# Performance work log

Measured on AMD Instinct MI355X. Metric: run time of the kernel, lower is better.

## Reference

```python
import jax, jax.numpy as jnp
import numpy as np

S, D_IN, N_RULES, N_OUT = 8192, 1024, 16, 512  # batch, in_features, num_rules, out_features


def setup_inputs() -> dict:
    key = jax.random.key(0)
    k1, k2, k3, k4 = jax.random.split(key, 4)
    X = jax.random.normal(k1, (S, D_IN), dtype=jnp.float32)
    # fc layer weight/bias after add_neurons: out_features = N_RULES * N_OUT
    W = jax.random.normal(k2, (N_RULES * N_OUT, D_IN), dtype=jnp.float32) / np.sqrt(D_IN).astype(np.float32)
    b = jax.random.normal(k3, (N_RULES * N_OUT,), dtype=jnp.float32) * 0.01
    # rule firing strengths from Layer (computed under no_grad in the original)
    lambdas = jax.random.uniform(k4, (S, N_RULES), dtype=jnp.float32)
    return {"X": X, "W": W, "b": b, "lambdas": lambdas}


def reference(X, W, b, lambdas):
    # X: [S, D_IN]; W: [R*O, D_IN]; b: [R*O]; lambdas: [S, R]
    H = jax.nn.sigmoid(X @ W.T + b)                       # [S, R*O]
    Hr = H.reshape(H.shape[0], lambdas.shape[1], N_OUT)   # [S, R, O] (block n = cols n*O:(n+1)*O)
    # apply_rule_strength: out[s,o] = sum_r lambdas[s,r] * H[s, r*O + o]
    return jnp.einsum('sr,sro->so', lambdas, Hr)          # [S, O]
```

## Files before the change

### kernel.cpp

```cpp
#include <hip/hip_runtime.h>
#include <hip/hip_bf16.h>
#include <stdint.h>

#define SS 8192
#define DD 1024
#define RR 16
#define OO 512

typedef __bf16 bf16_8 __attribute__((ext_vector_type(8)));
typedef float f32_4 __attribute__((ext_vector_type(4)));
typedef int i32_4 __attribute__((ext_vector_type(4)));

typedef __attribute__((address_space(1))) void g1_void;
typedef __attribute__((address_space(3))) void lds_void;

#define L2E 1.44269504f

__device__ __forceinline__ void gload_lds16(const void* g, void* l) {
  __builtin_amdgcn_global_load_lds((g1_void*)(uintptr_t)g,
                                   (lds_void*)(uint32_t)(uintptr_t)l, 16, 0, 0);
}

__global__ __launch_bounds__(256) void somfnn_quant(
    const float* __restrict__ X, const float* __restrict__ W,
    char* __restrict__ Xq, char* __restrict__ Wq,
    float* __restrict__ sX, float* __restrict__ sW, float4* __restrict__ out) {
  const int tid = threadIdx.x;
  const int wv = tid >> 6;
  const int l = tid & 63;
  const int r = blockIdx.x * 4 + wv;
  const bool isX = r < SS;
  const float* src = isX ? (X + (size_t)r * DD) : (W + (size_t)(r - SS) * DD);
  char* dst = isX ? (Xq + (size_t)r * DD) : (Wq + (size_t)(r - SS) * DD);

  const float4* s4 = (const float4*)src;
  float4 v[4];
#pragma unroll
  for (int c = 0; c < 4; ++c) v[c] = s4[c * 64 + l];

  out[(size_t)blockIdx.x * 256 + tid] = float4{0.f, 0.f, 0.f, 0.f};

  float m = 0.f;
#pragma unroll
  for (int c = 0; c < 4; ++c)
    m = fmaxf(m, fmaxf(fmaxf(fabsf(v[c].x), fabsf(v[c].y)),
                       fmaxf(fabsf(v[c].z), fabsf(v[c].w))));
#pragma unroll
  for (int off = 32; off > 0; off >>= 1) m = fmaxf(m, __shfl_xor(m, off, 64));
  m = fmaxf(m, 1e-20f);

  const float inv = 127.0f / m;
  int* di = (int*)dst;
#pragma unroll
  for (int c = 0; c < 4; ++c) {
    int q0 = __float2int_rn(v[c].x * inv);
    int q1 = __float2int_rn(v[c].y * inv);
    int q2 = __float2int_rn(v[c].z * inv);
    int q3 = __float2int_rn(v[c].w * inv);
    di[c * 64 + l] = (q0 & 0xff) | ((q1 & 0xff) << 8) | ((q2 & 0xff) << 16) |
                     ((q3 & 0xff) << 24);
  }
  if (l == 0) {
    if (isX) sX[r] = m / 127.0f;
    else sW[r - SS] = m / 127.0f;
  }
}

__global__ __launch_bounds__(256, 2) void somfnn_gemm_i8(
    const char* __restrict__ Xq, const char* __restrict__ Wq,
    const float* __restrict__ sX, const float* __restrict__ sW,
    const float* __restrict__ bias_g, const float* __restrict__ lam_g,
    float* __restrict__ out) {
  constexpr int BM = 128, BN = 128, BK = 128;
  constexpr int TILEB = BM * BK;
  constexpr int NSTEP = 8 * (DD / BK);

  __shared__ __align__(16) char lds_a[2][TILEB];
  __shared__ __align__(16) char lds_b[2][TILEB];
  __shared__ float lds_bias[8 * BN];
  __shared__ float lds_lam[8 * BM];
  __shared__ float lds_sB[8 * BN];
  __shared__ float lds_sA[BM];

  const int tid = threadIdx.x;
  const int bid = blockIdx.x;

  const int l = tid & 63;
  const int w = tid >> 6;
  const int lane15 = l & 15;
  const int q = l >> 4;
  const int wm = w >> 1;
  const int wn = w & 1;

  const int xcd = bid & 7;
  const int chunk = bid >> 3;
  const int sb = xcd * 8 + (chunk & 7);
  const int ob = (chunk >> 3) & 3;
  const int rhalf = chunk >> 5;
  const int s0 = sb * BM;
  const int o0 = ob * BN;
  const int r0 = rhalf * 8;

  for (int idx = tid; idx < 8 * BN; idx += 256) {
    int rr = idx >> 7, j = idx & 127;
    lds_bias[idx] = -L2E * bias_g[(r0 + rr) * OO + o0 + j];
    lds_sB[idx] = sW[(r0 + rr) * OO + o0 + j];
  }
  for (int idx = tid; idx < 8 * BM; idx += 256) {
    int rr = idx >> 7, i = idx & 127;
    lds_lam[idx] = lam_g[(s0 + i) * RR + (r0 + rr)];
  }
  if (tid < BM) lds_sA[tid] = sX[s0 + tid];

  int goffs[4];
#pragma unroll
  for (int i = 0; i < 4; ++i) {
    int c = (w * 4 + i) * 64 + l;
    int row = c >> 3;
    int k16 = (c & 7) ^ (row & 7);
    goffs[i] = row * DD + k16 * 16;
  }

  int afo[4], bfo[4];
#pragma unroll
  for (int t = 0; t < 4; ++t) {
    int ra = wm * 64 + t * 16 + lane15;
    afo[t] = ra * BK + ((q ^ (ra & 7)) * 16);
    int rb = wn * 64 + t * 16 + lane15;
    bfo[t] = rb * BK + ((q ^ (rb & 7)) * 16);
  }

  auto issue_pre = [&](int step, int buf) {
    int rl = step >> 3, kt = step & 7;
    const char* ga = Xq + (size_t)s0 * DD + kt * BK;
    const char* gb = Wq + ((size_t)(r0 + rl) * OO + o0) * DD + kt * BK;
#pragma unroll
    for (int i = 0; i < 4; ++i)
      gload_lds16(ga + goffs[i], &lds_a[buf][(w * 4 + i) * 1024]);
#pragma unroll
    for (int i = 0; i < 4; ++i)
      gload_lds16(gb + goffs[i], &lds_b[buf][(w * 4 + i) * 1024]);
  };

  i32_4 acc[4][4];
  f32_4 oacc[4][4];
#pragma unroll
  for (int mi = 0; mi < 4; ++mi)
#pragma unroll
    for (int ni = 0; ni < 4; ++ni) {
      acc[mi][ni] = i32_4{0, 0, 0, 0};
      oacc[mi][ni] = f32_4{0.f, 0.f, 0.f, 0.f};
    }

  issue_pre(0, 0);
  __syncthreads();

  for (int step = 0; step < NSTEP; ++step) {
    const int cur = step & 1;
    const bool more = (step + 1) < NSTEP;
    if (more) issue_pre(step + 1, cur ^ 1);

    const char* A = lds_a[cur];
    const char* B = lds_b[cur];
#pragma unroll
    for (int ks = 0; ks < 2; ++ks) {
      const int xr = ks ? 64 : 0;
      i32_4 av[4], bv[4];
#pragma unroll
      for (int mi = 0; mi < 4; ++mi) av[mi] = *(const i32_4*)(A + (afo[mi] ^ xr));
#pragma unroll
      for (int ni = 0; ni < 4; ++ni) bv[ni] = *(const i32_4*)(B + (bfo[ni] ^ xr));
#pragma unroll
      for (int mi = 0; mi < 4; ++mi)
#pragma unroll
        for (int ni = 0; ni < 4; ++ni)
          acc[mi][ni] =
              __builtin_amdgcn_mfma_i32_16x16x64_i8(av[mi], bv[ni], acc[mi][ni], 0, 0, 0);
    }

    if ((step & 7) == 7) {
      const int rl = step >> 3;
      float lsa[4][4], lamv[4][4];
#pragma unroll
      for (int mi = 0; mi < 4; ++mi)
#pragma unroll
        for (int v = 0; v < 4; ++v) {
          int ridx = wm * 64 + mi * 16 + q * 4 + v;
          lsa[mi][v] = -L2E * lds_sA[ridx];
          lamv[mi][v] = lds_lam[rl * BM + ridx];
        }
#pragma unroll
      for (int ni = 0; ni < 4; ++ni) {
        const int cidx = wn * 64 + ni * 16 + lane15;
        const float nb = lds_bias[rl * BN + cidx];
        const float sbv = lds_sB[rl * BN + cidx];
#pragma unroll
        for (int mi = 0; mi < 4; ++mi)
#pragma unroll
          for (int v = 0; v < 4; ++v) {
            float t = __builtin_fmaf((float)acc[mi][ni][v], lsa[mi][v] * sbv, nb);
            float e = __builtin_amdgcn_exp2f(t);
            float h = __builtin_amdgcn_rcpf(1.0f + e);
            oacc[mi][ni][v] = __builtin_fmaf(lamv[mi][v], h, oacc[mi][ni][v]);
            acc[mi][ni][v] = 0;
          }
      }
    }
    __syncthreads();
  }

#pragma unroll
  for (int mi = 0; mi < 4; ++mi)
#pragma unroll
    for (int ni = 0; ni < 4; ++ni)
#pragma unroll
      for (int v = 0; v < 4; ++v) {
        int row = s0 + wm * 64 + mi * 16 + q * 4 + v;
        int col = o0 + wn * 64 + ni * 16 + lane15;
        atomicAdd(&out[row * OO + col], oacc[mi][ni][v]);
      }
}

__global__ __launch_bounds__(256, 2) void somfnn_gemm_fb(
    const float* __restrict__ Xf32, const float* __restrict__ Wf32,
    const float* __restrict__ bias_g, const float* __restrict__ lam_g,
    float* __restrict__ out) {
  constexpr int BM = 128, BN = 128, BK = 64;
  constexpr int TILE = BM * BK;
  constexpr int NSTEP = 8 * (DD / BK);

  __shared__ __align__(16) __bf16 lds_a[2][TILE];
  __shared__ __align__(16) __bf16 lds_b[2][TILE];
  __shared__ float lds_bias[8 * BN];
  __shared__ float lds_lam[8 * BM];

  const int tid = threadIdx.x;
  const int bid = blockIdx.x;
  const int l = tid & 63;
  const int w = tid >> 6;
  const int lane15 = l & 15;
  const int q = l >> 4;
  const int wm = w >> 1;
  const int wn = w & 1;

  const int xcd = bid & 7;
  const int chunk = bid >> 3;
  const int sb = xcd * 8 + (chunk & 7);
  const int ob = (chunk >> 3) & 3;
  const int rhalf = chunk >> 5;
  const int s0 = sb * BM;
  const int o0 = ob * BN;
  const int r0 = rhalf * 8;

  for (int idx = tid; idx < 8 * BN; idx += 256) {
    int rr = idx >> 7, j = idx & 127;
    lds_bias[idx] = -L2E * bias_g[(r0 + rr) * OO + o0 + j];
  }
  for (int idx = tid; idx < 8 * BM; idx += 256) {
    int rr = idx >> 7, i = idx & 127;
    lds_lam[idx] = lam_g[(s0 + i) * RR + (r0 + rr)];
  }

  int goffs[4], coffs[4];
#pragma unroll
  for (int i = 0; i < 4; ++i) {
    int c = (w * 4 + i) * 64 + l;
    int row = c >> 3;
    int k8 = (c & 7) ^ (row & 7);
    goffs[i] = row * DD + k8 * 8;
    coffs[i] = c * 8;
  }
  int afo[4], bfo[4];
#pragma unroll
  for (int t = 0; t < 4; ++t) {
    int ra = wm * 64 + t * 16 + lane15;
    afo[t] = (ra * 8 + (q ^ (ra & 7))) * 8;
    int rb = wn * 64 + t * 16 + lane15;
    bfo[t] = (rb * 8 + (q ^ (rb & 7))) * 8;
  }

  float4 ra_[4][2], rb_[4][2];
  auto issue_fb = [&](int step) {
    int rl = step >> 4, kt = step & 15;
    const float* ga = Xf32 + s0 * DD + kt * BK;
    const float* gb = Wf32 + ((r0 + rl) * OO + o0) * DD + kt * BK;
#pragma unroll
    for (int i = 0; i < 4; ++i) {
      const float4* p = (const float4*)(ga + goffs[i]);
      ra_[i][0] = p[0]; ra_[i][1] = p[1];
      const float4* pb = (const float4*)(gb + goffs[i]);
      rb_[i][0] = pb[0]; rb_[i][1] = pb[1];
    }
  };
  auto commit_fb = [&](int buf) {
#pragma unroll
    for (int i = 0; i < 4; ++i) {
      bf16_8 t;
      t[0] = (__bf16)ra_[i][0].x; t[1] = (__bf16)ra_[i][0].y;
      t[2] = (__bf16)ra_[i][0].z; t[3] = (__bf16)ra_[i][0].w;
      t[4] = (__bf16)ra_[i][1].x; t[5] = (__bf16)ra_[i][1].y;
      t[6] = (__bf16)ra_[i][1].z; t[7] = (__bf16)ra_[i][1].w;
      *(bf16_8*)&lds_a[buf][coffs[i]] = t;
      bf16_8 u;
      u[0] = (__bf16)rb_[i][0].x; u[1] = (__bf16)rb_[i][0].y;
      u[2] = (__bf16)rb_[i][0].z; u[3] = (__bf16)rb_[i][0].w;
      u[4] = (__bf16)rb_[i][1].x; u[5] = (__bf16)rb_[i][1].y;
      u[6] = (__bf16)rb_[i][1].z; u[7] = (__bf16)rb_[i][1].w;
      *(bf16_8*)&lds_b[buf][coffs[i]] = u;
    }
  };

  f32_4 acc[4][4], oacc[4][4];
#pragma unroll
  for (int mi = 0; mi < 4; ++mi)
#pragma unroll
    for (int ni = 0; ni < 4; ++ni) {
      acc[mi][ni] = f32_4{0.f, 0.f, 0.f, 0.f};
      oacc[mi][ni] = f32_4{0.f, 0.f, 0.f, 0.f};
    }

  issue_fb(0);
  commit_fb(0);
  __syncthreads();

  for (int step = 0; step < NSTEP; ++step) {
    const int cur = step & 1;
    const bool more = (step + 1) < NSTEP;
    if (more) issue_fb(step + 1);

    const __bf16* A = lds_a[cur];
    const __bf16* B = lds_b[cur];
#pragma unroll
    for (int ks = 0; ks < 2; ++ks) {
      const int xr = ks ? 32 : 0;
      bf16_8 av[4], bv[4];
#pragma unroll
      for (int mi = 0; mi < 4; ++mi) av[mi] = *(const bf16_8*)(A + (afo[mi] ^ xr));
#pragma unroll
      for (int ni = 0; ni < 4; ++ni) bv[ni] = *(const bf16_8*)(B + (bfo[ni] ^ xr));
#pragma unroll
      for (int mi = 0; mi < 4; ++mi)
#pragma unroll
        for (int ni = 0; ni < 4; ++ni)
          acc[mi][ni] =
              __builtin_amdgcn_mfma_f32_16x16x32_bf16(av[mi], bv[ni], acc[mi][ni], 0, 0, 0);
    }
    if (more) commit_fb(cur ^ 1);

    if ((step & 15) == 15) {
      const int rl = step >> 4;
      float lamv[4][4];
#pragma unroll
      for (int mi = 0; mi < 4; ++mi)
#pragma unroll
        for (int v = 0; v < 4; ++v)
          lamv[mi][v] = lds_lam[rl * BM + wm * 64 + mi * 16 + q * 4 + v];
#pragma unroll
      for (int ni = 0; ni < 4; ++ni) {
        const float nb = lds_bias[rl * BN + wn * 64 + ni * 16 + lane15];
#pragma unroll
        for (int mi = 0; mi < 4; ++mi)
#pragma unroll
          for (int v = 0; v < 4; ++v) {
            float t = __builtin_fmaf(acc[mi][ni][v], -L2E, nb);
            float e = __builtin_amdgcn_exp2f(t);
            float h = __builtin_amdgcn_rcpf(1.0f + e);
            oacc[mi][ni][v] = __builtin_fmaf(lamv[mi][v], h, oacc[mi][ni][v]);
            acc[mi][ni][v] = 0.f;
          }
      }
    }
    __syncthreads();
  }

#pragma unroll
  for (int mi = 0; mi < 4; ++mi)
#pragma unroll
    for (int ni = 0; ni < 4; ++ni)
#pragma unroll
      for (int v = 0; v < 4; ++v) {
        int row = s0 + wm * 64 + mi * 16 + q * 4 + v;
        int col = o0 + wn * 64 + ni * 16 + lane15;
        atomicAdd(&out[row * OO + col], oacc[mi][ni][v]);
      }
}

extern "C" void kernel_launch(void* const* d_in, const int* in_sizes, int n_in,
                              void* d_out, int out_size, void* d_ws, size_t ws_size,
                              hipStream_t stream) {
  const float* X = (const float*)d_in[0];
  const float* W = (const float*)d_in[1];
  const float* b = (const float*)d_in[2];
  const float* lam = (const float*)d_in[3];
  float* out = (float*)d_out;

  const size_t qbytes = (size_t)SS * DD;
  const size_t need = 2 * qbytes + 2 * (size_t)SS * sizeof(float);
  if (ws_size >= need) {
    char* Xq = (char*)d_ws;
    char* Wq = Xq + qbytes;
    float* sX = (float*)(Wq + qbytes);
    float* sW = sX + SS;
    somfnn_quant<<<dim3(4096), dim3(256), 0, stream>>>(X, W, Xq, Wq, sX, sW, (float4*)out);
    somfnn_gemm_i8<<<dim3(512), dim3(256), 0, stream>>>(Xq, Wq, sX, sW, b, lam, out);
  } else {
    hipMemsetAsync(out, 0, (size_t)SS * OO * sizeof(float), stream);
    somfnn_gemm_fb<<<dim3(512), dim3(256), 0, stream>>>(X, W, b, lam, out);
  }
}
```

Baseline: 199.4 us.

## Reuse each X tile across two rules per K step with dual accumulators

The int8 GEMM now processes two rules at once. It loads one 64-wide K slice of the X tile and W tiles for two rules, then runs MFMAs into two separate accumulator sets. This halves how often the X tile is reloaded into LDS and held in registers across the 8 rules, at the cost of twice the accumulator registers and a new swizzle for the narrower BK. The added register pressure could spill or lower occupancy under launch_bounds(256,2).

```diff
diff --git a/kernel.cpp b/kernel.cpp
--- a/kernel.cpp
+++ b/kernel.cpp
@@ -71,12 +71,13 @@
     const float* __restrict__ sX, const float* __restrict__ sW,
     const float* __restrict__ bias_g, const float* __restrict__ lam_g,
     float* __restrict__ out) {
-  constexpr int BM = 128, BN = 128, BK = 128;
+  constexpr int BM = 128, BN = 128, BK = 64;
   constexpr int TILEB = BM * BK;
-  constexpr int NSTEP = 8 * (DD / BK);
+  constexpr int KT = DD / BK;
+  constexpr int NSTEP = 4 * KT;
 
   __shared__ __align__(16) char lds_a[2][TILEB];
-  __shared__ __align__(16) char lds_b[2][TILEB];
+  __shared__ __align__(16) char lds_b[2][2][TILEB];
   __shared__ float lds_bias[8 * BN];
   __shared__ float lds_lam[8 * BM];
   __shared__ float lds_sB[8 * BN];
@@ -112,48 +113,81 @@
   }
   if (tid < BM) lds_sA[tid] = sX[s0 + tid];
 
-  int goffs[4];
-#pragma unroll
-  for (int i = 0; i < 4; ++i) {
-    int c = (w * 4 + i) * 64 + l;
-    int row = c >> 3;
-    int k16 = (c & 7) ^ (row & 7);
-    goffs[i] = row * DD + k16 * 16;
+  int goffs[2];
+#pragma unroll
+  for (int i = 0; i < 2; ++i) {
+    int cc = (w * 2 + i) * 64 + l;
+    int row = cc >> 2;
+    int lc = cc & 3;
+    goffs[i] = row * DD + ((lc ^ ((row >> 1) & 3)) * 16);
   }
 
   int afo[4], bfo[4];
 #pragma unroll
   for (int t = 0; t < 4; ++t) {
     int ra = wm * 64 + t * 16 + lane15;
-    afo[t] = ra * BK + ((q ^ (ra & 7)) * 16);
+    afo[t] = ra * BK + ((q ^ ((ra >> 1) & 3)) * 16);
     int rb = wn * 64 + t * 16 + lane15;
-    bfo[t] = rb * BK + ((q ^ (rb & 7)) * 16);
+    bfo[t] = rb * BK + ((q ^ ((rb >> 1) & 3)) * 16);
   }
 
   auto issue_pre = [&](int step, int buf) {
-    int rl = step >> 3, kt = step & 7;
+    int rp = step >> 4, kt = step & 15;
     const char* ga = Xq + (size_t)s0 * DD + kt * BK;
-    const char* gb = Wq + ((size_t)(r0 + rl) * OO + o0) * DD + kt * BK;
-#pragma unroll
-    for (int i = 0; i < 4; ++i)
-      gload_lds16(ga + goffs[i], &lds_a[buf][(w * 4 + i) * 1024]);
-#pragma unroll
-    for (int i = 0; i < 4; ++i)
-      gload_lds16(gb + goffs[i], &lds_b[buf][(w * 4 + i) * 1024]);
+    const char* gb0 = Wq + ((size_t)(r0 + 2 * rp) * OO + o0) * DD + kt * BK;
+    const char* gb1 = gb0 + (size_t)OO * DD;
+#pragma unroll
+    for (int i = 0; i < 2; ++i)
+      gload_lds16(ga + goffs[i], &lds_a[buf][(w * 2 + i) * 1024]);
+#pragma unroll
+    for (int i = 0; i < 2; ++i)
+      gload_lds16(gb0 + goffs[i], &lds_b[buf][0][(w * 2 + i) * 1024]);
+#pragma unroll
+    for (int i = 0; i < 2; ++i)
+      gload_lds16(gb1 + goffs[i], &lds_b[buf][1][(w * 2 + i) * 1024]);
   };
 
-  i32_4 acc[4][4];
+  i32_4 acc0[4][4], acc1[4][4];
   f32_4 oacc[4][4];
 #pragma unroll
   for (int mi = 0; mi < 4; ++mi)
 #pragma unroll
     for (int ni = 0; ni < 4; ++ni) {
-      acc[mi][ni] = i32_4{0, 0, 0, 0};
+      acc0[mi][ni] = i32_4{0, 0, 0, 0};
+      acc1[mi][ni] = i32_4{0, 0, 0, 0};
       oacc[mi][ni] = f32_4{0.f, 0.f, 0.f, 0.f};
     }
 
   issue_pre(0, 0);
   __syncthreads();
+
+  auto do_epi = [&](i32_4 (&ac)[4][4], int rr) {
+    float lsa[4][4], lamv[4][4];
+#pragma unroll
+    for (int mi = 0; mi < 4; ++mi)
+#pragma unroll
+      for (int v = 0; v < 4; ++v) {
+        int ridx = wm * 64 + mi * 16 + q * 4 + v;
+        lsa[mi][v] = -L2E * lds_sA[ridx];
+        lamv[mi][v] = lds_lam[rr * BM + ridx];
+      }
+#pragma unroll
+    for (int ni = 0; ni < 4; ++ni) {
+      const int cidx = wn * 64 + ni * 16 + lane15;
+      const float nb = lds_bias[rr * BN + cidx];
+      const float sbv = lds_sB[rr * BN + cidx];
+#pragma unroll
+      for (int mi = 0; mi < 4; ++mi)
+#pragma unroll
+        for (int v = 0; v < 4; ++v) {
+          float t = __builtin_fmaf((float)ac[mi][ni][v], lsa[mi][v] * sbv, nb);
+          float e = __builtin_amdgcn_exp2f(t);
+          float h = __builtin_amdgcn_rcpf(1.0f + e);
+          oacc[mi][ni][v] = __builtin_fmaf(lamv[mi][v], h, oacc[mi][ni][v]);
+          ac[mi][ni][v] = 0;
+        }
+    }
+  };
 
   for (int step = 0; step < NSTEP; ++step) {
     const int cur = step & 1;
@@ -161,50 +195,33 @@
     if (more) issue_pre(step + 1, cur ^ 1);
 
     const char* A = lds_a[cur];
-    const char* B = lds_b[cur];
-#pragma unroll
-    for (int ks = 0; ks < 2; ++ks) {
-      const int xr = ks ? 64 : 0;
-      i32_4 av[4], bv[4];
-#pragma unroll
-      for (int mi = 0; mi < 4; ++mi) av[mi] = *(const i32_4*)(A + (afo[mi] ^ xr));
-#pragma unroll
-      for (int ni = 0; ni < 4; ++ni) bv[ni] = *(const i32_4*)(B + (bfo[ni] ^ xr));
-#pragma unroll
-      for (int mi = 0; mi < 4; ++mi)
-#pragma unroll
-        for (int ni = 0; ni < 4; ++ni)
-          acc[mi][ni] =
-              __builtin_amdgcn_mfma_i32_16x16x64_i8(av[mi], bv[ni], acc[mi][ni], 0, 0, 0);
-    }
-
-    if ((step & 7) == 7) {
-      const int rl = step >> 3;
-      float lsa[4][4], lamv[4][4];
-#pragma unroll
-      for (int mi = 0; mi < 4; ++mi)
-#pragma unroll
-        for (int v = 0; v < 4; ++v) {
-          int ridx = wm * 64 + mi * 16 + q * 4 + v;
-          lsa[mi][v] = -L2E * lds_sA[ridx];
-          lamv[mi][v] = lds_lam[rl * BM + ridx];
-        }
-#pragma unroll
-      for (int ni = 0; ni < 4; ++ni) {
-        const int cidx = wn * 64 + ni * 16 + lane15;
-        const float nb = lds_bias[rl * BN + cidx];
-        const float sbv = lds_sB[rl * BN + cidx];
-#pragma unroll
-        for (int mi = 0; mi < 4; ++mi)
-#pragma unroll
-          for (int v = 0; v < 4; ++v) {
-            float t = __builtin_fmaf((float)acc[mi][ni][v], lsa[mi][v] * sbv, nb);
-            float e = __builtin_amdgcn_exp2f(t);
-            float h = __builtin_amdgcn_rcpf(1.0f + e);
-            oacc[mi][ni][v] = __builtin_fmaf(lamv[mi][v], h, oacc[mi][ni][v]);
-            acc[mi][ni][v] = 0;
-          }
-      }
+    const char* B0 = lds_b[cur][0];
+    const char* B1 = lds_b[cur][1];
+
+    i32_4 av[4], bv[4];
+#pragma unroll
+    for (int mi = 0; mi < 4; ++mi) av[mi] = *(const i32_4*)(A + afo[mi]);
+#pragma unroll
+    for (int ni = 0; ni < 4; ++ni) bv[ni] = *(const i32_4*)(B0 + bfo[ni]);
+#pragma unroll
+    for (int mi = 0; mi < 4; ++mi)
+#pragma unroll
+      for (int ni = 0; ni < 4; ++ni)
+        acc0[mi][ni] =
+            __builtin_amdgcn_mfma_i32_16x16x64_i8(av[mi], bv[ni], acc0[mi][ni], 0, 0, 0);
+#pragma unroll
+    for (int ni = 0; ni < 4; ++ni) bv[ni] = *(const i32_4*)(B1 + bfo[ni]);
+#pragma unroll
+    for (int mi = 0; mi < 4; ++mi)
+#pragma unroll
+      for (int ni = 0; ni < 4; ++ni)
+        acc1[mi][ni] =
+            __builtin_amdgcn_mfma_i32_16x16x64_i8(av[mi], bv[ni], acc1[mi][ni], 0, 0, 0);
+
+    if ((step & 15) == 15) {
+      const int rp = step >> 4;
+      do_epi(acc0, 2 * rp);
+      do_epi(acc1, 2 * rp + 1);
     }
     __syncthreads();
   }
```

After: 197.9 us. Within noise of the previous version (-0.8%).

## Use triple-buffered BK=64 pipeline with partial vmcnt waits in int8 GEMM

Applied to the files above, without the earlier changes.

Halves the K tile to 64 and moves from double to triple buffering of the LDS tiles, issuing loads two steps ahead. The full __syncthreads is replaced by s_waitcnt vmcnt(4) plus a raw s_barrier, so the next stage's loads stay in flight across the barrier. The LDS swizzle is adjusted for the narrower 64-byte rows. The intent is to hide global-to-LDS latency better, at the cost of twice as many barriers and a smaller MFMA batch per step.

```diff
diff --git a/kernel.cpp b/kernel.cpp
--- a/kernel.cpp
+++ b/kernel.cpp
@@ -71,12 +71,12 @@
     const float* __restrict__ sX, const float* __restrict__ sW,
     const float* __restrict__ bias_g, const float* __restrict__ lam_g,
     float* __restrict__ out) {
-  constexpr int BM = 128, BN = 128, BK = 128;
+  constexpr int BM = 128, BN = 128, BK = 64;
   constexpr int TILEB = BM * BK;
   constexpr int NSTEP = 8 * (DD / BK);
 
-  __shared__ __align__(16) char lds_a[2][TILEB];
-  __shared__ __align__(16) char lds_b[2][TILEB];
+  __shared__ __align__(16) char lds_a[3][TILEB];
+  __shared__ __align__(16) char lds_b[3][TILEB];
   __shared__ float lds_bias[8 * BN];
   __shared__ float lds_lam[8 * BM];
   __shared__ float lds_sB[8 * BN];
@@ -112,34 +112,34 @@
   }
   if (tid < BM) lds_sA[tid] = sX[s0 + tid];
 
-  int goffs[4];
-#pragma unroll
-  for (int i = 0; i < 4; ++i) {
-    int c = (w * 4 + i) * 64 + l;
-    int row = c >> 3;
-    int k16 = (c & 7) ^ (row & 7);
-    goffs[i] = row * DD + k16 * 16;
+  int goffs[2];
+#pragma unroll
+  for (int i = 0; i < 2; ++i) {
+    int cc = (w * 2 + i) * 64 + l;
+    int row = cc >> 2;
+    int lc = cc & 3;
+    goffs[i] = row * DD + ((lc ^ ((row >> 1) & 3)) * 16);
   }
 
   int afo[4], bfo[4];
 #pragma unroll
   for (int t = 0; t < 4; ++t) {
     int ra = wm * 64 + t * 16 + lane15;
-    afo[t] = ra * BK + ((q ^ (ra & 7)) * 16);
+    afo[t] = ra * BK + ((q ^ ((ra >> 1) & 3)) * 16);
     int rb = wn * 64 + t * 16 + lane15;
-    bfo[t] = rb * BK + ((q ^ (rb & 7)) * 16);
+    bfo[t] = rb * BK + ((q ^ ((rb >> 1) & 3)) * 16);
   }
 
   auto issue_pre = [&](int step, int buf) {
-    int rl = step >> 3, kt = step & 7;
+    int rl = step >> 4, kt = step & 15;
     const char* ga = Xq + (size_t)s0 * DD + kt * BK;
     const char* gb = Wq + ((size_t)(r0 + rl) * OO + o0) * DD + kt * BK;
 #pragma unroll
-    for (int i = 0; i < 4; ++i)
-      gload_lds16(ga + goffs[i], &lds_a[buf][(w * 4 + i) * 1024]);
-#pragma unroll
-    for (int i = 0; i < 4; ++i)
-      gload_lds16(gb + goffs[i], &lds_b[buf][(w * 4 + i) * 1024]);
+    for (int i = 0; i < 2; ++i)
+      gload_lds16(ga + goffs[i], &lds_a[buf][(w * 2 + i) * 1024]);
+#pragma unroll
+    for (int i = 0; i < 2; ++i)
+      gload_lds16(gb + goffs[i], &lds_b[buf][(w * 2 + i) * 1024]);
   };
 
   i32_4 acc[4][4];
@@ -152,34 +152,35 @@
       oacc[mi][ni] = f32_4{0.f, 0.f, 0.f, 0.f};
     }
 
+  asm volatile("s_waitcnt vmcnt(0)" ::: "memory");
   issue_pre(0, 0);
-  __syncthreads();
+  issue_pre(1, 1);
+  asm volatile("s_waitcnt vmcnt(4) lgkmcnt(0)" ::: "memory");
+  __builtin_amdgcn_sched_barrier(0);
+  __builtin_amdgcn_s_barrier();
+  __builtin_amdgcn_sched_barrier(0);
 
   for (int step = 0; step < NSTEP; ++step) {
-    const int cur = step & 1;
-    const bool more = (step + 1) < NSTEP;
-    if (more) issue_pre(step + 1, cur ^ 1);
+    const int cur = step % 3;
+    const bool more = (step + 2) < NSTEP;
+    if (more) issue_pre(step + 2, (step + 2) % 3);
 
     const char* A = lds_a[cur];
     const char* B = lds_b[cur];
-#pragma unroll
-    for (int ks = 0; ks < 2; ++ks) {
-      const int xr = ks ? 64 : 0;
-      i32_4 av[4], bv[4];
-#pragma unroll
-      for (int mi = 0; mi < 4; ++mi) av[mi] = *(const i32_4*)(A + (afo[mi] ^ xr));
-#pragma unroll
-      for (int ni = 0; ni < 4; ++ni) bv[ni] = *(const i32_4*)(B + (bfo[ni] ^ xr));
-#pragma unroll
-      for (int mi = 0; mi < 4; ++mi)
-#pragma unroll
-        for (int ni = 0; ni < 4; ++ni)
-          acc[mi][ni] =
-              __builtin_amdgcn_mfma_i32_16x16x64_i8(av[mi], bv[ni], acc[mi][ni], 0, 0, 0);
-    }
-
-    if ((step & 7) == 7) {
-      const int rl = step >> 3;
+    i32_4 av[4], bv[4];
+#pragma unroll
+    for (int mi = 0; mi < 4; ++mi) av[mi] = *(const i32_4*)(A + afo[mi]);
+#pragma unroll
+    for (int ni = 0; ni < 4; ++ni) bv[ni] = *(const i32_4*)(B + bfo[ni]);
+#pragma unroll
+    for (int mi = 0; mi < 4; ++mi)
+#pragma unroll
+      for (int ni = 0; ni < 4; ++ni)
+        acc[mi][ni] =
+            __builtin_amdgcn_mfma_i32_16x16x64_i8(av[mi], bv[ni], acc[mi][ni], 0, 0, 0);
+
+    if ((step & 15) == 15) {
+      const int rl = step >> 4;
       float lsa[4][4], lamv[4][4];
 #pragma unroll
       for (int mi = 0; mi < 4; ++mi)
@@ -206,7 +207,15 @@
           }
       }
     }
-    __syncthreads();
+
+    if (more) {
+      asm volatile("s_waitcnt vmcnt(4) lgkmcnt(0)" ::: "memory");
+    } else {
+      asm volatile("s_waitcnt vmcnt(0) lgkmcnt(0)" ::: "memory");
+    }
+    __builtin_amdgcn_sched_barrier(0);
+    __builtin_amdgcn_s_barrier();
+    __builtin_amdgcn_sched_barrier(0);
   }
 
 #pragma unroll
```

Result: slower. 204.4 us (+2.5%).

## Give each wave private LDS tiles and drop block-wide barriers in int8 GEMM loop

Applied to the files above, without the earlier changes.

The int8 GEMM now has each wave load its own 64-row A and B slices into a private double-buffered LDS region, with BK shrunk to 64. The per-step __syncthreads is replaced by explicit vmcnt/lgkmcnt waits, so waves run independently and keep two loads in flight. The aim is to remove block-wide barrier stalls and overlap loads with MFMA. In exchange, the four waves no longer share loads, so global/L2 traffic per block roughly doubles, and correctness depends on the hand-written waitcnt ordering.

```diff
diff --git a/kernel.cpp b/kernel.cpp
--- a/kernel.cpp
+++ b/kernel.cpp
@@ -71,12 +71,10 @@
     const float* __restrict__ sX, const float* __restrict__ sW,
     const float* __restrict__ bias_g, const float* __restrict__ lam_g,
     float* __restrict__ out) {
-  constexpr int BM = 128, BN = 128, BK = 128;
-  constexpr int TILEB = BM * BK;
-  constexpr int NSTEP = 8 * (DD / BK);
-
-  __shared__ __align__(16) char lds_a[2][TILEB];
-  __shared__ __align__(16) char lds_b[2][TILEB];
+  constexpr int BM = 128, BN = 128;
+  constexpr int NSTEP = 8 * 16;
+
+  __shared__ __align__(16) char lds_t[4][2][8192];
   __shared__ float lds_bias[8 * BN];
   __shared__ float lds_lam[8 * BM];
   __shared__ float lds_sB[8 * BN];
@@ -112,34 +110,35 @@
   }
   if (tid < BM) lds_sA[tid] = sX[s0 + tid];
 
-  int goffs[4];
+  int arow_off[4];
 #pragma unroll
   for (int i = 0; i < 4; ++i) {
-    int c = (w * 4 + i) * 64 + l;
-    int row = c >> 3;
-    int k16 = (c & 7) ^ (row & 7);
-    goffs[i] = row * DD + k16 * 16;
-  }
-
-  int afo[4], bfo[4];
+    int s = 64 * i + l;
+    int r = ((s >> 4) << 2) | (s & 3);
+    int kc = ((s >> 2) & 3) ^ ((s >> 4) & 3);
+    arow_off[i] = r * DD + kc * 16;
+  }
+
+  int afo[4];
 #pragma unroll
   for (int t = 0; t < 4; ++t) {
-    int ra = wm * 64 + t * 16 + lane15;
-    afo[t] = ra * BK + ((q ^ (ra & 7)) * 16);
-    int rb = wn * 64 + t * 16 + lane15;
-    bfo[t] = rb * BK + ((q ^ (rb & 7)) * 16);
-  }
-
-  auto issue_pre = [&](int step, int buf) {
-    int rl = step >> 3, kt = step & 7;
-    const char* ga = Xq + (size_t)s0 * DD + kt * BK;
-    const char* gb = Wq + ((size_t)(r0 + rl) * OO + o0) * DD + kt * BK;
-#pragma unroll
-    for (int i = 0; i < 4; ++i)
-      gload_lds16(ga + goffs[i], &lds_a[buf][(w * 4 + i) * 1024]);
-#pragma unroll
-    for (int i = 0; i < 4; ++i)
-      gload_lds16(gb + goffs[i], &lds_b[buf][(w * 4 + i) * 1024]);
+    int r = t * 16 + lane15;
+    afo[t] = (r >> 2) * 256 + ((q ^ ((r >> 2) & 3)) * 64) + ((r & 3) * 16);
+  }
+
+  const char* gAbase = Xq + (size_t)(s0 + wm * 64) * DD;
+  const char* gBbase = Wq + ((size_t)r0 * OO + o0 + wn * 64) * DD;
+  char* lds_w = &lds_t[w][0][0];
+
+  auto issue = [&](int it, int buf) {
+    int rl = it >> 4, kt = it & 15;
+    const char* ga = gAbase + kt * 64;
+    const char* gb = gBbase + (size_t)rl * OO * DD + kt * 64;
+    char* la = lds_w + buf * 8192;
+#pragma unroll
+    for (int i = 0; i < 4; ++i) gload_lds16(ga + arow_off[i], la + i * 1024);
+#pragma unroll
+    for (int i = 0; i < 4; ++i) gload_lds16(gb + arow_off[i], la + 4096 + i * 1024);
   };
 
   i32_4 acc[4][4];
@@ -152,34 +151,36 @@
       oacc[mi][ni] = f32_4{0.f, 0.f, 0.f, 0.f};
     }
 
-  issue_pre(0, 0);
   __syncthreads();
 
-  for (int step = 0; step < NSTEP; ++step) {
-    const int cur = step & 1;
-    const bool more = (step + 1) < NSTEP;
-    if (more) issue_pre(step + 1, cur ^ 1);
-
-    const char* A = lds_a[cur];
-    const char* B = lds_b[cur];
-#pragma unroll
-    for (int ks = 0; ks < 2; ++ks) {
-      const int xr = ks ? 64 : 0;
-      i32_4 av[4], bv[4];
-#pragma unroll
-      for (int mi = 0; mi < 4; ++mi) av[mi] = *(const i32_4*)(A + (afo[mi] ^ xr));
-#pragma unroll
-      for (int ni = 0; ni < 4; ++ni) bv[ni] = *(const i32_4*)(B + (bfo[ni] ^ xr));
-#pragma unroll
-      for (int mi = 0; mi < 4; ++mi)
-#pragma unroll
-        for (int ni = 0; ni < 4; ++ni)
-          acc[mi][ni] =
-              __builtin_amdgcn_mfma_i32_16x16x64_i8(av[mi], bv[ni], acc[mi][ni], 0, 0, 0);
-    }
-
-    if ((step & 7) == 7) {
-      const int rl = step >> 3;
+  issue(0, 0);
+  issue(1, 1);
+
+  for (int it = 0; it < NSTEP; ++it) {
+    const int cur = it & 1;
+
+    if (it + 1 < NSTEP) {
+      asm volatile("s_waitcnt vmcnt(8)" ::: "memory");
+    } else {
+      asm volatile("s_waitcnt vmcnt(0)" ::: "memory");
+    }
+    __builtin_amdgcn_sched_barrier(0);
+
+    const char* A = lds_w + cur * 8192;
+    i32_4 av[4], bv[4];
+#pragma unroll
+    for (int mi = 0; mi < 4; ++mi) av[mi] = *(const i32_4*)(A + afo[mi]);
+#pragma unroll
+    for (int ni = 0; ni < 4; ++ni) bv[ni] = *(const i32_4*)(A + 4096 + afo[ni]);
+#pragma unroll
+    for (int mi = 0; mi < 4; ++mi)
+#pragma unroll
+      for (int ni = 0; ni < 4; ++ni)
+        acc[mi][ni] =
+            __builtin_amdgcn_mfma_i32_16x16x64_i8(av[mi], bv[ni], acc[mi][ni], 0, 0, 0);
+
+    if ((it & 15) == 15) {
+      const int rl = it >> 4;
       float lsa[4][4], lamv[4][4];
 #pragma unroll
       for (int mi = 0; mi < 4; ++mi)
@@ -206,7 +207,12 @@
           }
       }
     }
-    __syncthreads();
+
+    if (it + 2 < NSTEP) {
+      asm volatile("s_waitcnt lgkmcnt(0)" ::: "memory");
+      __builtin_amdgcn_sched_barrier(0);
+      issue(it + 2, cur);
+    }
   }
 
 #pragma unroll
```

After: 348.7 us. 1.75x slower.
